# Kernel optimization log

Measured on AMD Instinct MI355X. Metric: run time of the kernel, lower is better.

## Reference

```python
import jax, jax.numpy as jnp
import numpy as np

N_CLASS = 32000
N_HIDDEN = 1024
ENC_LEN = 512
DEC_LEN = 256


def setup_inputs() -> dict:
    key = jax.random.key(0)
    ks = jax.random.split(key, 12)
    s = 0.02
    return {
        "enc_input": jax.random.normal(ks[0], (1, ENC_LEN, N_CLASS), jnp.float32),
        "hidden": jnp.zeros((1, 1, N_HIDDEN), jnp.float32),
        "dec_input": jax.random.normal(ks[1], (1, DEC_LEN, N_CLASS), jnp.float32),
        "enc_W_ih": jax.random.normal(ks[2], (N_HIDDEN, N_CLASS), jnp.float32) * s,
        "enc_W_hh": jax.random.normal(ks[3], (N_HIDDEN, N_HIDDEN), jnp.float32) * s,
        "enc_b_ih": jnp.zeros((N_HIDDEN,), jnp.float32),
        "enc_b_hh": jnp.zeros((N_HIDDEN,), jnp.float32),
        "dec_W_ih": jax.random.normal(ks[4], (N_HIDDEN, N_CLASS), jnp.float32) * s,
        "dec_W_hh": jax.random.normal(ks[5], (N_HIDDEN, N_HIDDEN), jnp.float32) * s,
        "dec_b_ih": jnp.zeros((N_HIDDEN,), jnp.float32),
        "dec_b_hh": jnp.zeros((N_HIDDEN,), jnp.float32),
        "attn_W": jax.random.normal(ks[6], (N_HIDDEN, N_HIDDEN), jnp.float32) * s,
        "attn_b": jnp.zeros((N_HIDDEN,), jnp.float32),
        "out_W": jax.random.normal(ks[7], (N_CLASS, 2 * N_HIDDEN), jnp.float32) * s,
        "out_b": jnp.zeros((N_CLASS,), jnp.float32),
    }


def _rnn_scan(x_seq, h0, W_ih, W_hh, b_ih, b_hh):
    # x_seq: [S, in], h0: [H]. Vanilla tanh RNN, batch=1 (vectors).
    xw = x_seq @ W_ih.T + b_ih  # precompute input projections [S, H]

    def step(h, xw_t):
        h_new = jnp.tanh(xw_t + h @ W_hh.T + b_hh)
        return h_new, h_new

    h_last, outs = jax.lax.scan(step, h0, xw)
    return outs, h_last


def reference(enc_input, hidden, dec_input,
              enc_W_ih, enc_W_hh, enc_b_ih, enc_b_hh,
              dec_W_ih, dec_W_hh, dec_b_ih, dec_b_hh,
              attn_W, attn_b, out_W, out_b):
    x_enc = enc_input[0]  # [S_enc, n_class] (batch=1)
    x_dec = dec_input[0]  # [S_dec, n_class]
    h0 = hidden[0, 0]     # [H]

    enc_outputs, h_enc = _rnn_scan(x_enc, h0, enc_W_ih, enc_W_hh, enc_b_ih, enc_b_hh)

    # attn Linear applied to encoder outputs once: scores_i = dec_h . attn(enc_i)
    A = enc_outputs @ attn_W.T + attn_b  # [S_enc, H]

    xw_dec = x_dec @ dec_W_ih.T + dec_b_ih  # [S_dec, H]

    def dec_step(h, xw_t):
        h_new = jnp.tanh(xw_t + h @ dec_W_hh.T + dec_b_hh)
        scores = A @ h_new                    # [S_enc]
        w = jax.nn.softmax(scores)            # [S_enc]
        context = w @ enc_outputs             # [H]
        o = jnp.concatenate([h_new, context]) @ out_W.T + out_b  # [n_class]
        return h_new, (o, w)

    _, (outs, attns) = jax.lax.scan(dec_step, h_enc, xw_dec)
    # outs: [S_dec, n_class] == model.transpose(0,1).squeeze(0)
    # attns: [S_dec, S_enc] == stacked trained_attn
    return outs, attns
```

## Files before the change

kernel.cpp:

```cpp
#include <hip/hip_runtime.h>
#include <hip/hip_fp16.h>
#include <math.h>

#define S_ENC 512
#define S_DEC 256
#define HID   1024
#define NCLS  32000
#define KOUT  2048

typedef _Float16 f16;
typedef _Float16 f16x8 __attribute__((ext_vector_type(8)));
typedef _Float16 f16x4 __attribute__((ext_vector_type(4)));
typedef float    f32x4 __attribute__((ext_vector_type(4)));

__device__ __forceinline__ f16x8 cvt8(float4 a, float4 b) {
  f16x8 r;
  r[0] = (f16)a.x; r[1] = (f16)a.y; r[2] = (f16)a.z; r[3] = (f16)a.w;
  r[4] = (f16)b.x; r[5] = (f16)b.y; r[6] = (f16)b.z; r[7] = (f16)b.w;
  return r;
}

__global__ __launch_bounds__(256, 2)
void gemm_nt_part(const float* __restrict__ A, const float* __restrict__ B,
                  float* __restrict__ P, int M, int N, int K, int KC)
{
  __shared__ f16x8 As8[256 * 4];
  __shared__ f16x8 Bs8[64 * 4];
  const int tid  = threadIdx.x;
  const int lane = tid & 63;
  const int wv   = tid >> 6;
  const int m0 = blockIdx.x << 8;
  const int n0 = blockIdx.y << 6;
  const int k0 = blockIdx.z * KC;

  f32x4 acc[4][4];
#pragma unroll
  for (int p = 0; p < 4; ++p)
#pragma unroll
    for (int f = 0; f < 4; ++f)
      acc[p][f] = (f32x4){0.f, 0.f, 0.f, 0.f};

  const int swa  = (tid >> 1) & 3;
  const int brow = tid & 63;
  const int bq   = tid >> 6;
  const int swb  = (brow >> 1) & 3;
  const int q    = lane >> 4;
  const int rl   = lane & 15;

  for (int kk = k0; kk < k0 + KC; kk += 32) {
    const float4* sa = (const float4*)(A + (size_t)(m0 + tid) * K + kk);
    float4 av[8];
#pragma unroll
    for (int j = 0; j < 8; ++j) av[j] = sa[j];
    const float4* sb = (const float4*)(B + (size_t)(n0 + brow) * K + kk);
    float4 bv0 = sb[2 * bq];
    float4 bv1 = sb[2 * bq + 1];
#pragma unroll
    for (int g = 0; g < 4; ++g)
      As8[(tid << 2) + (g ^ swa)] = cvt8(av[2 * g], av[2 * g + 1]);
    Bs8[(brow << 2) + (bq ^ swb)] = cvt8(bv0, bv1);
    __syncthreads();

    f16x8 af[4], bf[4];
#pragma unroll
    for (int p = 0; p < 4; ++p) {
      int r = (wv << 6) + (p << 4) + rl;
      af[p] = As8[(r << 2) + (q ^ ((r >> 1) & 3))];
    }
#pragma unroll
    for (int f = 0; f < 4; ++f) {
      int c = (f << 4) + rl;
      bf[f] = Bs8[(c << 2) + (q ^ ((c >> 1) & 3))];
    }
#pragma unroll
    for (int p = 0; p < 4; ++p)
#pragma unroll
      for (int f = 0; f < 4; ++f)
        acc[p][f] = __builtin_amdgcn_mfma_f32_16x16x32_f16(af[p], bf[f], acc[p][f], 0, 0, 0);
    __syncthreads();
  }

  float* Pz = P + (size_t)blockIdx.z * M * N;
#pragma unroll
  for (int p = 0; p < 4; ++p)
#pragma unroll
    for (int i = 0; i < 4; ++i) {
      int row = m0 + (wv << 6) + (p << 4) + (q << 2) + i;
      float* dst = Pz + (size_t)row * N + n0 + rl;
#pragma unroll
      for (int f = 0; f < 4; ++f)
        dst[f << 4] = acc[p][f][i];
    }
}

__global__ __launch_bounds__(256, 2)
void gemm_out_f16(const f16* __restrict__ A16, const float* __restrict__ B,
                  const float* __restrict__ bias, float* __restrict__ C)
{
  __shared__ f16x8 As8[256 * 4];
  __shared__ f16x8 Bs8[64 * 4];
  const int tid  = threadIdx.x;
  const int lane = tid & 63;
  const int wv   = tid >> 6;
  const int n0   = blockIdx.x << 6;

  f32x4 acc[4][4];
#pragma unroll
  for (int p = 0; p < 4; ++p)
#pragma unroll
    for (int f = 0; f < 4; ++f)
      acc[p][f] = (f32x4){0.f, 0.f, 0.f, 0.f};

  const int swa  = (tid >> 1) & 3;
  const int brow = tid & 63;
  const int bq   = tid >> 6;
  const int swb  = (brow >> 1) & 3;
  const int q    = lane >> 4;
  const int rl   = lane & 15;

  for (int kk = 0; kk < KOUT; kk += 32) {
    const uint4* sa = (const uint4*)(A16 + (size_t)tid * KOUT + kk);
    uint4 av[4];
#pragma unroll
    for (int g = 0; g < 4; ++g) av[g] = sa[g];
    const float4* sb = (const float4*)(B + (size_t)(n0 + brow) * KOUT + kk);
    float4 bv0 = sb[2 * bq];
    float4 bv1 = sb[2 * bq + 1];
#pragma unroll
    for (int g = 0; g < 4; ++g)
      ((uint4*)As8)[(tid << 2) + (g ^ swa)] = av[g];
    Bs8[(brow << 2) + (bq ^ swb)] = cvt8(bv0, bv1);
    __syncthreads();

    f16x8 af[4], bf[4];
#pragma unroll
    for (int p = 0; p < 4; ++p) {
      int r = (wv << 6) + (p << 4) + rl;
      af[p] = As8[(r << 2) + (q ^ ((r >> 1) & 3))];
    }
#pragma unroll
    for (int f = 0; f < 4; ++f) {
      int c = (f << 4) + rl;
      bf[f] = Bs8[(c << 2) + (q ^ ((c >> 1) & 3))];
    }
#pragma unroll
    for (int p = 0; p < 4; ++p)
#pragma unroll
      for (int f = 0; f < 4; ++f)
        acc[p][f] = __builtin_amdgcn_mfma_f32_16x16x32_f16(af[p], bf[f], acc[p][f], 0, 0, 0);
    __syncthreads();
  }

  float bv[4];
#pragma unroll
  for (int f = 0; f < 4; ++f) bv[f] = bias[n0 + (f << 4) + rl];
#pragma unroll
  for (int p = 0; p < 4; ++p)
#pragma unroll
    for (int i = 0; i < 4; ++i) {
      int row = (wv << 6) + (p << 4) + (q << 2) + i;
      float* dst = C + (size_t)row * NCLS + n0 + rl;
#pragma unroll
      for (int f = 0; f < 4; ++f)
        dst[f << 4] = acc[p][f][i] + bv[f];
    }
}

__global__ void reduce_bias(const float* __restrict__ P, const float* __restrict__ bias,
                            float* __restrict__ out, int MN, int Z)
{
  int idx = blockIdx.x * 256 + threadIdx.x;
  if (idx >= MN) return;
  float s = bias[idx & (HID - 1)];
  for (int z = 0; z < Z; ++z) s += P[(size_t)z * MN + idx];
  out[idx] = s;
}

__global__ void init_flags(int* __restrict__ f) { f[threadIdx.x] = 0; }

__device__ __forceinline__ int hcpos(int g) { return (g ^ ((g >> 3) & 7)) << 2; }

__global__ __launch_bounds__(256)
void rnn_scan(const float* __restrict__ Whh, const float* __restrict__ bhh,
              const float* __restrict__ xw, const float* __restrict__ h0,
              float* __restrict__ Eout, f16* __restrict__ H16,
              float* __restrict__ hbuf, int* __restrict__ flags, int T)
{
  __shared__ float hc[HID];
  const int tid  = threadIdx.x;
  const int lane = tid & 63;
  const int wv   = tid >> 6;
  const int wid  = blockIdx.x;
  const int rbase = (wid << 4) + (wv << 2);

  float4 W[4][4];
#pragma unroll
  for (int rr = 0; rr < 4; ++rr)
#pragma unroll
    for (int g = 0; g < 4; ++g)
      W[rr][g] = *(const float4*)(Whh + (size_t)(rbase + rr) * HID + (lane << 4) + (g << 2));

  const int myrow = rbase + lane;
  float mybias = (lane < 4) ? bhh[myrow] : 0.f;

  *(float4*)(hc + hcpos(tid)) = *(const float4*)(h0 + (tid << 2));
  __syncthreads();

  for (int t = 0; t < T; ++t) {
    float4 hv[4];
#pragma unroll
    for (int g = 0; g < 4; ++g)
      hv[g] = *(const float4*)(hc + hcpos((lane << 2) + g));
    float p[4];
#pragma unroll
    for (int rr = 0; rr < 4; ++rr) {
      float s = 0.f;
#pragma unroll
      for (int g = 0; g < 4; ++g) {
        s = fmaf(W[rr][g].x, hv[g].x, s);
        s = fmaf(W[rr][g].y, hv[g].y, s);
        s = fmaf(W[rr][g].z, hv[g].z, s);
        s = fmaf(W[rr][g].w, hv[g].w, s);
      }
      p[rr] = s;
    }
#pragma unroll
    for (int d = 32; d >= 1; d >>= 1) {
#pragma unroll
      for (int rr = 0; rr < 4; ++rr)
        p[rr] += __shfl_xor(p[rr], d);
    }
    if (lane < 4) {
      float z = p[lane] + xw[(size_t)t * HID + myrow] + mybias;
      float h = tanhf(z);
      __hip_atomic_store(hbuf + (((t + 1) & 1) << 10) + myrow, h,
                         __ATOMIC_RELAXED, __HIP_MEMORY_SCOPE_AGENT);
      if (Eout) Eout[(size_t)t * HID + myrow] = h;
      if (H16)  H16[(size_t)t * KOUT + myrow] = (f16)h;
    }
    __syncthreads();
    if (tid == 0)
      __hip_atomic_store(&flags[wid << 2], t + 1, __ATOMIC_RELEASE, __HIP_MEMORY_SCOPE_AGENT);
    if (wv == 0) {
      while (__hip_atomic_load(&flags[lane << 2], __ATOMIC_ACQUIRE,
                               __HIP_MEMORY_SCOPE_AGENT) <= t) {}
    }
    __syncthreads();
    *(float4*)(hc + hcpos(tid)) =
        *(const float4*)(hbuf + (((t + 1) & 1) << 10) + (tid << 2));
    __syncthreads();
  }
}

__global__ __launch_bounds__(256, 4)
void attn_scores(const f16* __restrict__ HC16, const float* __restrict__ Abuf,
                 float* __restrict__ attns, float* __restrict__ wbuf)
{
  __shared__ float h[HID];
  __shared__ float red[8];
  const int t = blockIdx.x;
  const int tid = threadIdx.x;
  const int lane = tid & 63;
  const int wv = tid >> 6;
  {
    f16x4 v = *(const f16x4*)(HC16 + (size_t)t * KOUT + (tid << 2));
    float4 f;
    f.x = (float)v[0]; f.y = (float)v[1]; f.z = (float)v[2]; f.w = (float)v[3];
    *(float4*)(h + (tid << 2)) = f;
  }
  __syncthreads();
  float s0 = 0.f, s1 = 0.f;
  {
    const float4* A0 = (const float4*)(Abuf + (size_t)tid * HID);
    const float4* A1 = (const float4*)(Abuf + (size_t)(tid + 256) * HID);
    float a0x = 0, a0y = 0, a0z = 0, a0w = 0, a1x = 0, a1y = 0, a1z = 0, a1w = 0;
#pragma unroll 8
    for (int j = 0; j < 256; ++j) {
      float4 hv = *(const float4*)(h + (j << 2));
      float4 a0 = A0[j];
      float4 a1 = A1[j];
      a0x = fmaf(a0.x, hv.x, a0x); a0y = fmaf(a0.y, hv.y, a0y);
      a0z = fmaf(a0.z, hv.z, a0z); a0w = fmaf(a0.w, hv.w, a0w);
      a1x = fmaf(a1.x, hv.x, a1x); a1y = fmaf(a1.y, hv.y, a1y);
      a1z = fmaf(a1.z, hv.z, a1z); a1w = fmaf(a1.w, hv.w, a1w);
    }
    s0 = (a0x + a0y) + (a0z + a0w);
    s1 = (a1x + a1y) + (a1z + a1w);
  }
  float m = fmaxf(s0, s1);
#pragma unroll
  for (int d = 32; d >= 1; d >>= 1) m = fmaxf(m, __shfl_xor(m, d));
  if (lane == 0) red[wv] = m;
  __syncthreads();
  float M = fmaxf(fmaxf(red[0], red[1]), fmaxf(red[2], red[3]));
  float e0 = expf(s0 - M);
  float e1 = expf(s1 - M);
  float ss = e0 + e1;
#pragma unroll
  for (int d = 32; d >= 1; d >>= 1) ss += __shfl_xor(ss, d);
  if (lane == 0) red[4 + wv] = ss;
  __syncthreads();
  float inv = 1.f / (red[4] + red[5] + red[6] + red[7]);
  float w0 = e0 * inv, w1 = e1 * inv;
  attns[(size_t)t * S_ENC + tid]       = w0;
  attns[(size_t)t * S_ENC + 256 + tid] = w1;
  wbuf[(size_t)t * S_ENC + tid]        = w0;
  wbuf[(size_t)t * S_ENC + 256 + tid]  = w1;
}

__global__ __launch_bounds__(256, 4)
void attn_context(const float* __restrict__ wbuf, const float* __restrict__ E,
                  f16* __restrict__ HC16)
{
  __shared__ float w[S_ENC];
  const int t = blockIdx.x;
  const int tid = threadIdx.x;
  w[tid]       = wbuf[(size_t)t * S_ENC + tid];
  w[tid + 256] = wbuf[(size_t)t * S_ENC + 256 + tid];
  __syncthreads();
  float ax = 0, ay = 0, az = 0, aw = 0;
  const float4* Eb = (const float4*)E + tid;
#pragma unroll 4
  for (int i = 0; i < S_ENC; ++i) {
    float wi = w[i];
    float4 e = Eb[(size_t)i * 256];
    ax = fmaf(wi, e.x, ax); ay = fmaf(wi, e.y, ay);
    az = fmaf(wi, e.z, az); aw = fmaf(wi, e.w, aw);
  }
  f16x4 o;
  o[0] = (f16)ax; o[1] = (f16)ay; o[2] = (f16)az; o[3] = (f16)aw;
  *(f16x4*)(HC16 + (size_t)t * KOUT + HID + (tid << 2)) = o;
}

extern "C" void kernel_launch(void* const* d_in, const int* in_sizes, int n_in,
                              void* d_out, int out_size, void* d_ws, size_t ws_size,
                              hipStream_t stream)
{
  const float* enc_input = (const float*)d_in[0];
  const float* hidden    = (const float*)d_in[1];
  const float* dec_input = (const float*)d_in[2];
  const float* enc_W_ih  = (const float*)d_in[3];
  const float* enc_W_hh  = (const float*)d_in[4];
  const float* enc_b_ih  = (const float*)d_in[5];
  const float* enc_b_hh  = (const float*)d_in[6];
  const float* dec_W_ih  = (const float*)d_in[7];
  const float* dec_W_hh  = (const float*)d_in[8];
  const float* dec_b_ih  = (const float*)d_in[9];
  const float* dec_b_hh  = (const float*)d_in[10];
  const float* attn_W    = (const float*)d_in[11];
  const float* attn_b    = (const float*)d_in[12];
  const float* out_W     = (const float*)d_in[13];
  const float* out_b     = (const float*)d_in[14];

  float* outs  = (float*)d_out;
  float* attns = (float*)d_out + (size_t)S_DEC * NCLS;

  float* wsf     = (float*)d_ws;
  float* xw_enc  = wsf + 0;
  float* xw_dec  = wsf + 524288;
  float* Abuf    = wsf + 786432;
  float* E       = wsf + 1310720;
  float* wbuf    = wsf + 1835008;
  float* hbuf_e  = wsf + 1966080;
  float* hbuf_d  = wsf + 1968128;
  int*   flags   = (int*)(wsf + 1970176);
  f16*   HC16    = (f16*)(wsf + 1971200);
  float* P_enc   = wsf + 2233344;
  float* P_dec   = wsf + 6427648;
  float* P_A     = P_enc;

  init_flags<<<1, 1024, 0, stream>>>(flags);

  gemm_nt_part<<<dim3(2, 16, 8), 256, 0, stream>>>(enc_input, enc_W_ih, P_enc,
                                                   S_ENC, HID, NCLS, 4000);
  gemm_nt_part<<<dim3(1, 16, 8), 256, 0, stream>>>(dec_input, dec_W_ih, P_dec,
                                                   S_DEC, HID, NCLS, 4000);
  reduce_bias<<<2048, 256, 0, stream>>>(P_enc, enc_b_ih, xw_enc, S_ENC * HID, 8);
  reduce_bias<<<1024, 256, 0, stream>>>(P_dec, dec_b_ih, xw_dec, S_DEC * HID, 8);

  rnn_scan<<<64, 256, 0, stream>>>(enc_W_hh, enc_b_hh, xw_enc, hidden,
                                   E, (f16*)nullptr, hbuf_e, flags, S_ENC);

  gemm_nt_part<<<dim3(2, 16, 4), 256, 0, stream>>>(E, attn_W, P_A,
                                                   S_ENC, HID, HID, 256);
  reduce_bias<<<2048, 256, 0, stream>>>(P_A, attn_b, Abuf, S_ENC * HID, 4);

  rnn_scan<<<64, 256, 0, stream>>>(dec_W_hh, dec_b_hh, xw_dec, E + 511 * HID,
                                   (float*)nullptr, HC16, hbuf_d, flags + 256, S_DEC);

  attn_scores<<<256, 256, 0, stream>>>(HC16, Abuf, attns, wbuf);
  attn_context<<<256, 256, 0, stream>>>(wbuf, E, HC16);
  gemm_out_f16<<<500, 256, 0, stream>>>(HC16, out_W, out_b, outs);

  (void)in_sizes; (void)n_in; (void)out_size; (void)ws_size;
}
```

Measured before the change: 4.076 ms.

## Replace flag barrier in RNN scan with tagged fp16 hidden-state words

```diff
diff --git a/kernel.cpp b/kernel.cpp
--- a/kernel.cpp
+++ b/kernel.cpp
@@ -176,7 +176,9 @@
   out[idx] = s;
 }
 
-__global__ void init_flags(int* __restrict__ f) { f[threadIdx.x] = 0; }
+__global__ void init_hx(unsigned int* __restrict__ hx) {
+  ((uint4*)hx)[threadIdx.x] = (uint4){0u, 0u, 0u, 0u};
+}
 
 __device__ __forceinline__ int hcpos(int g) { return (g ^ ((g >> 3) & 7)) << 2; }
 
@@ -184,7 +186,7 @@
 void rnn_scan(const float* __restrict__ Whh, const float* __restrict__ bhh,
               const float* __restrict__ xw, const float* __restrict__ h0,
               float* __restrict__ Eout, f16* __restrict__ H16,
-              float* __restrict__ hbuf, int* __restrict__ flags, int T)
+              unsigned int* __restrict__ hx, int T)
 {
   __shared__ float hc[HID];
   const int tid  = threadIdx.x;
@@ -207,6 +209,8 @@
   __syncthreads();
 
   for (int t = 0; t < T; ++t) {
+    float xwv = (lane < 4) ? xw[(size_t)t * HID + myrow] : 0.f;
+
     float4 hv[4];
 #pragma unroll
     for (int g = 0; g < 4; ++g)
@@ -230,25 +234,39 @@
       for (int rr = 0; rr < 4; ++rr)
         p[rr] += __shfl_xor(p[rr], d);
     }
+
+    const unsigned int tag = (unsigned int)(t + 1);
+    const int par = (t + 1) & 1;
+
     if (lane < 4) {
-      float z = p[lane] + xw[(size_t)t * HID + myrow] + mybias;
+      float z = p[lane] + xwv + mybias;
       float h = tanhf(z);
-      __hip_atomic_store(hbuf + (((t + 1) & 1) << 10) + myrow, h,
+      if (Eout) Eout[(size_t)t * HID + myrow] = h;
+      f16 h16 = (f16)h;
+      if (H16)  H16[(size_t)t * KOUT + myrow] = h16;
+      unsigned int wword = (tag << 16) | (unsigned int)__builtin_bit_cast(unsigned short, h16);
+      __hip_atomic_store(hx + (par << 10) + myrow, wword,
                          __ATOMIC_RELAXED, __HIP_MEMORY_SCOPE_AGENT);
-      if (Eout) Eout[(size_t)t * HID + myrow] = h;
-      if (H16)  H16[(size_t)t * KOUT + myrow] = (f16)h;
-    }
-    __syncthreads();
-    if (tid == 0)
-      __hip_atomic_store(&flags[wid << 2], t + 1, __ATOMIC_RELEASE, __HIP_MEMORY_SCOPE_AGENT);
-    if (wv == 0) {
-      while (__hip_atomic_load(&flags[lane << 2], __ATOMIC_ACQUIRE,
-                               __HIP_MEMORY_SCOPE_AGENT) <= t) {}
-    }
-    __syncthreads();
-    *(float4*)(hc + hcpos(tid)) =
-        *(const float4*)(hbuf + (((t + 1) & 1) << 10) + (tid << 2));
-    __syncthreads();
+    }
+
+    if (t + 1 < T) {
+      unsigned int* bp = hx + (par << 10) + (tid << 2);
+      unsigned int a0, a1, a2, a3;
+      do {
+        a0 = __hip_atomic_load(bp + 0, __ATOMIC_RELAXED, __HIP_MEMORY_SCOPE_AGENT);
+        a1 = __hip_atomic_load(bp + 1, __ATOMIC_RELAXED, __HIP_MEMORY_SCOPE_AGENT);
+        a2 = __hip_atomic_load(bp + 2, __ATOMIC_RELAXED, __HIP_MEMORY_SCOPE_AGENT);
+        a3 = __hip_atomic_load(bp + 3, __ATOMIC_RELAXED, __HIP_MEMORY_SCOPE_AGENT);
+      } while (((a0 >> 16) != tag) | ((a1 >> 16) != tag) |
+               ((a2 >> 16) != tag) | ((a3 >> 16) != tag));
+      float4 f;
+      f.x = (float)__builtin_bit_cast(f16, (unsigned short)(a0 & 0xFFFFu));
+      f.y = (float)__builtin_bit_cast(f16, (unsigned short)(a1 & 0xFFFFu));
+      f.z = (float)__builtin_bit_cast(f16, (unsigned short)(a2 & 0xFFFFu));
+      f.w = (float)__builtin_bit_cast(f16, (unsigned short)(a3 & 0xFFFFu));
+      *(float4*)(hc + hcpos(tid)) = f;
+      __syncthreads();
+    }
   }
 }
 
@@ -361,15 +379,14 @@
   float* Abuf    = wsf + 786432;
   float* E       = wsf + 1310720;
   float* wbuf    = wsf + 1835008;
-  float* hbuf_e  = wsf + 1966080;
-  float* hbuf_d  = wsf + 1968128;
-  int*   flags   = (int*)(wsf + 1970176);
-  f16*   HC16    = (f16*)(wsf + 1971200);
-  float* P_enc   = wsf + 2233344;
-  float* P_dec   = wsf + 6427648;
+  unsigned int* hx_e = (unsigned int*)(wsf + 1966080);
+  unsigned int* hx_d = hx_e + 2048;
+  f16*   HC16    = (f16*)(wsf + 1970176);
+  float* P_enc   = wsf + 2232320;
+  float* P_dec   = wsf + 6426624;
   float* P_A     = P_enc;
 
-  init_flags<<<1, 1024, 0, stream>>>(flags);
+  init_hx<<<1, 1024, 0, stream>>>(hx_e);
 
   gemm_nt_part<<<dim3(2, 16, 8), 256, 0, stream>>>(enc_input, enc_W_ih, P_enc,
                                                    S_ENC, HID, NCLS, 4000);
@@ -379,14 +396,14 @@
   reduce_bias<<<1024, 256, 0, stream>>>(P_dec, dec_b_ih, xw_dec, S_DEC * HID, 8);
 
   rnn_scan<<<64, 256, 0, stream>>>(enc_W_hh, enc_b_hh, xw_enc, hidden,
-                                   E, (f16*)nullptr, hbuf_e, flags, S_ENC);
+                                   E, (f16*)nullptr, hx_e, S_ENC);
 
   gemm_nt_part<<<dim3(2, 16, 4), 256, 0, stream>>>(E, attn_W, P_A,
                                                    S_ENC, HID, HID, 256);
   reduce_bias<<<2048, 256, 0, stream>>>(P_A, attn_b, Abuf, S_ENC * HID, 4);
 
   rnn_scan<<<64, 256, 0, stream>>>(dec_W_hh, dec_b_hh, xw_dec, E + 511 * HID,
-                                   (float*)nullptr, HC16, hbuf_d, flags + 256, S_DEC);
+                                   (float*)nullptr, HC16, hx_d, S_DEC);
 
   attn_scores<<<256, 256, 0, stream>>>(HC16, Abuf, attns, wbuf);
   attn_context<<<256, 256, 0, stream>>>(wbuf, E, HC16);
```

Result: faster. 3.549 ms (-12.9%).
